# Kernel optimization log

Hardware: AMD Instinct MI355X
Metric: run time of the kernel (lower is better)

The kernel has to match this reference:

```python
import jax, jax.numpy as jnp
import numpy as np

NMS_THRE = 0.4
NEG = -1e30  # sentinel for sort key of suppressed boxes


def _iou_adjacency(boxes, nms_thre):
    # boxes: [N,4] in cxcywh -> xyxy, then dense IoU >= thre adjacency (no self loops)
    cx, cy, w, h = boxes[:, 0], boxes[:, 1], boxes[:, 2], boxes[:, 3]
    x1 = cx - w / 2
    y1 = cy - h / 2
    x2 = x1 + w
    y2 = y1 + h
    b = jnp.stack([x1, y1, x2, y2], axis=-1)  # [N,4]
    area = (x2 - x1) * (y2 - y1)
    lt = jnp.maximum(b[:, None, :2], b[None, :, :2])  # [N,N,2]
    rb = jnp.minimum(b[:, None, 2:], b[None, :, 2:])
    wh = jnp.clip(rb - lt, 0.0)
    inter = wh[..., 0] * wh[..., 1]
    iou = inter / (area[:, None] + area[None, :] - inter)
    n = boxes.shape[0]
    return (iou >= nms_thre) & (~jnp.eye(n, dtype=bool))


def _greedy_suppress(valid0, adj, scores):
    # Sequential greedy NMS over candidates in descending score order.
    # valid shrinks monotonically, and valid <= valid0 always, so clearing
    # neighbors via adj row exactly matches the torch loop (which only clears
    # neighbors that were initially valid -- already-false entries are no-ops).
    order = jnp.argsort(-scores)

    def body(k, valid):
        idx = order[k]
        return jnp.where(valid[idx], valid & (~adj[idx]), valid)

    return jax.lax.fori_loop(0, scores.shape[0], body, valid0)


def _per_class(pro_c, con_c, conf_c, adj):
    # scatter_max over adjacency: max of con over neighbors (0 if no neighbors,
    # matching torch_scatter's zero-init)
    adj_con = jnp.max(jnp.where(adj, con_c[None, :], 0.0), axis=1)
    valid0 = (pro_c >= conf_c) & (pro_c >= adj_con) & (pro_c >= con_c)
    return _greedy_suppress(valid0, adj, pro_c)


def _per_image(pro, con, boxes, scale, conf_thres):
    # pro/con: [N,C]; boxes: [N,4] cxcywh; scale: scalar; conf_thres: [C]
    adj = _iou_adjacency(boxes, NMS_THRE)
    survive = jax.vmap(_per_class, in_axes=(1, 1, 0, None))(pro, con, conf_thres, adj)  # [C,N]
    b = boxes * scale
    cx, cy, w, h = b[:, 0], b[:, 1], b[:, 2], b[:, 3]
    xyxy = jnp.stack([cx - 0.5 * w, cy - 0.5 * h, cx + 0.5 * w, cy + 0.5 * h], axis=-1)  # [N,4]
    scores = pro.T  # [C,N]
    C = scores.shape[0]
    bws = jnp.concatenate(
        [jnp.broadcast_to(xyxy[None], (C,) + xyxy.shape), scores[..., None]], axis=-1
    )  # [C,N,5]
    bws = bws * survive[..., None].astype(bws.dtype)  # zero out suppressed rows
    key = jnp.where(survive, scores, NEG)
    perm = jnp.argsort(-key, axis=1)  # per-class descending score order
    bws = jnp.take_along_axis(bws, perm[..., None], axis=1)
    mask = jnp.take_along_axis(survive, perm, axis=1)
    return bws, mask


def setup_inputs() -> dict:
    key = jax.random.key(0)
    k1, k2, k3, k4 = jax.random.split(key, 4)
    B, N, C = 4, 3600, 16
    return {
        "pro_max": jax.random.uniform(k1, (B, N, C), dtype=jnp.float32),
        "con_max": jax.random.uniform(k2, (B, N, C), dtype=jnp.float32),
        "pred_boxes": jax.random.uniform(k3, (B, N, 4), dtype=jnp.float32),
        "image_scales": jax.random.uniform(k4, (B,), dtype=jnp.float32),
        "conf_thres": jnp.zeros((C,), dtype=jnp.float32),
    }


def reference(pro_max, con_max, pred_boxes, image_scales, conf_thres):
    # Returns (boxes_with_scores [B,C,N,5] sorted per class by score desc,
    #          survive_mask [B,C,N] aligned with the sorted rows).
    return jax.vmap(_per_image, in_axes=(0, 0, 0, 0, None))(
        pro_max, con_max, pred_boxes, image_scales, conf_thres
    )
```

## Files before the change

kernel.cpp:

```cpp
#include <hip/hip_runtime.h>
#include <cstdint>

typedef unsigned long long u64;
typedef unsigned int u32;

#define B_ 4
#define N_ 3600
#define C_ 16
#define NW_ 57
#define NPAD_ 3648
#define RPW_ 4
#define RPB_ 16
#define HW0_ 1856
#define HW1_ 1792
#define CH_ 64
#define NT_ 512
#define NWV_ 8
#define RPWG_ 8

__global__ __launch_bounds__(256, 4) void k_adj(const float* __restrict__ boxes,
                                                const float* __restrict__ con,
                                                u64* __restrict__ adj,
                                                float* __restrict__ thr) {
#pragma clang fp contract(off)
    __shared__ float4 sbox[HW0_];
    const int tid  = threadIdx.x;
    const int lane = tid & 63;
    const int wv   = tid >> 6;
    const int g    = blockIdx.x;
    const int b    = g / (N_ / RPB_);
    const int r0   = (g % (N_ / RPB_)) * RPB_ + wv * RPW_;
    const size_t bN = (size_t)b * N_;

    float4 bi[RPW_];
    float  ai[RPW_];
#pragma unroll
    for (int r = 0; r < RPW_; ++r) {
        const float4 bx = reinterpret_cast<const float4*>(boxes)[bN + r0 + r];
        const float x1 = bx.x - bx.z * 0.5f;
        const float y1 = bx.y - bx.w * 0.5f;
        const float x2 = x1 + bx.z;
        const float y2 = y1 + bx.w;
        bi[r] = make_float4(x1, y1, x2, y2);
        ai[r] = (x2 - x1) * (y2 - y1);
    }
    const double MID = (double)0.4f - 0x1p-26;

    u64 row[RPW_];
#pragma unroll
    for (int r = 0; r < RPW_; ++r) row[r] = 0ull;

    int jbase = 0;
    for (int h = 0; h < 2; ++h) {
        const int cnt = h ? HW1_ : HW0_;
        __syncthreads();
        for (int jj = tid; jj < cnt; jj += 256) {
            const int j = jbase + jj;
            float x1 = 0.f, y1 = 0.f, x2 = 0.f, y2 = 0.f;
            if (j < N_) {
                const float4 bx = reinterpret_cast<const float4*>(boxes)[bN + j];
                x1 = bx.x - bx.z * 0.5f;
                y1 = bx.y - bx.w * 0.5f;
                x2 = x1 + bx.z;
                y2 = y1 + bx.w;
            }
            sbox[jj] = make_float4(x1, y1, x2, y2);
        }
        __syncthreads();

        const int twn = cnt >> 6;
        for (int tw = 0; tw < twn; ++tw) {
            const int tglob = (jbase >> 6) + tw;
            const int j     = jbase + tw * 64 + lane;
            const float4 bj = sbox[tw * 64 + lane];
            const float ajr = (bj.z - bj.x) * (bj.w - bj.y);
#pragma unroll
            for (int r = 0; r < RPW_; ++r) {
                const float ltx = fmaxf(bi[r].x, bj.x);
                const float lty = fmaxf(bi[r].y, bj.y);
                const float rbx = fminf(bi[r].z, bj.z);
                const float rby = fminf(bi[r].w, bj.w);
                const float whx = fmaxf(rbx - ltx, 0.0f);
                const float why = fmaxf(rby - lty, 0.0f);
                const float inter = whx * why;
                const float denom = (ai[r] + ajr) - inter;
                const int pred = ((double)inter > MID * (double)denom) && (j != r0 + r);
                const u64 m = __ballot(pred);
                if (lane == tglob) row[r] = m;
            }
        }
        jbase += cnt;
    }

#pragma unroll
    for (int r = 0; r < RPW_; ++r)
        if (lane < NW_) adj[(bN + r0 + r) * (size_t)NW_ + lane] = row[r];

#pragma unroll 1
    for (int r = 0; r < RPW_; ++r) {
        const int i = r0 + r;
        u64 w = row[r];
        float cm[C_];
#pragma unroll
        for (int k = 0; k < C_; ++k) cm[k] = 0.0f;

        while (w) {
            const int bit = __builtin_ctzll(w); w &= w - 1;
            const int j   = lane * 64 + bit;
            const float4* cp = reinterpret_cast<const float4*>(con + (bN + j) * C_);
            const float4 c0 = cp[0], c1 = cp[1], c2 = cp[2], c3 = cp[3];
            cm[0]  = fmaxf(cm[0],  c0.x); cm[1]  = fmaxf(cm[1],  c0.y);
            cm[2]  = fmaxf(cm[2],  c0.z); cm[3]  = fmaxf(cm[3],  c0.w);
            cm[4]  = fmaxf(cm[4],  c1.x); cm[5]  = fmaxf(cm[5],  c1.y);
            cm[6]  = fmaxf(cm[6],  c1.z); cm[7]  = fmaxf(cm[7],  c1.w);
            cm[8]  = fmaxf(cm[8],  c2.x); cm[9]  = fmaxf(cm[9],  c2.y);
            cm[10] = fmaxf(cm[10], c2.z); cm[11] = fmaxf(cm[11], c2.w);
            cm[12] = fmaxf(cm[12], c3.x); cm[13] = fmaxf(cm[13], c3.y);
            cm[14] = fmaxf(cm[14], c3.z); cm[15] = fmaxf(cm[15], c3.w);
        }

#pragma unroll
        for (int off = 1; off < 64; off <<= 1) {
#pragma unroll
            for (int k = 0; k < C_; ++k) cm[k] = fmaxf(cm[k], __shfl_xor(cm[k], off));
        }
        if (lane == 0) {
            const float4* cp = reinterpret_cast<const float4*>(con + (bN + i) * C_);
            const float4 c0 = cp[0], c1 = cp[1], c2 = cp[2], c3 = cp[3];
            float4* o = reinterpret_cast<float4*>(thr + (bN + i) * C_);
            o[0] = make_float4(fmaxf(cm[0],  c0.x), fmaxf(cm[1],  c0.y),
                               fmaxf(cm[2],  c0.z), fmaxf(cm[3],  c0.w));
            o[1] = make_float4(fmaxf(cm[4],  c1.x), fmaxf(cm[5],  c1.y),
                               fmaxf(cm[6],  c1.z), fmaxf(cm[7],  c1.w));
            o[2] = make_float4(fmaxf(cm[8],  c2.x), fmaxf(cm[9],  c2.y),
                               fmaxf(cm[10], c2.z), fmaxf(cm[11], c2.w));
            o[3] = make_float4(fmaxf(cm[12], c3.x), fmaxf(cm[13], c3.y),
                               fmaxf(cm[14], c3.z), fmaxf(cm[15], c3.w));
        }
    }
}

union OvT {
    u64 keys[NPAD_];
    u64 srows[2][CH_][NW_];
};

__global__ __launch_bounds__(NT_) void k_nms(const float* __restrict__ pro,
                                             const float* __restrict__ thr,
                                             const float* __restrict__ conf,
                                             const u64* __restrict__ adj,
                                             const float* __restrict__ boxes,
                                             const float* __restrict__ scales,
                                             float* __restrict__ out) {
#pragma clang fp contract(off)
    __shared__ OvT ov;
    __shared__ u32 sidx[NPAD_];
    __shared__ u64 sintra[CH_];
    __shared__ u64 vmask[NW_];
    __shared__ u64 s_accept;
    __shared__ u32 slist[NPAD_];
    __shared__ u32 s_T;
    __shared__ u32 s_S;
    const int tid  = threadIdx.x;
    const int lane = tid & 63;
    const int wv   = tid >> 6;
    const int bc   = blockIdx.x;
    const int b    = bc / C_, c = bc % C_;
    const size_t bN = (size_t)b * N_;
    const float cf = conf[c];

    if (tid == 0) s_T = 0;
    __syncthreads();

    for (int t = wv; t < NW_; t += NWV_) {
        const int i = t * 64 + lane;
        int pred = 0;
        u32 pk = 0;
        if (i < N_) {
            const size_t off = (bN + i) * C_ + c;
            const float p = pro[off];
            pred = (p >= cf) && (p >= thr[off]);
            const u32 pb = __float_as_uint(p);
            pk = pb ^ ((pb >> 31) ? 0xFFFFFFFFu : 0x80000000u);
        }
        const u64 bm = __ballot(pred);
        if (lane == 0) vmask[t] = bm;
        u32 base = 0;
        if (lane == 0 && bm) base = atomicAdd(&s_T, (u32)__popcll(bm));
        base = (u32)__shfl((int)base, 0);
        if (pred) ov.keys[base + (u32)__popcll(bm & ((1ull << lane) - 1ull))] =
            (((u64)(~pk)) << 32) | (u32)i;
    }
    __syncthreads();

    const int T = (int)s_T;
    for (int k = 0; k * NT_ < T; ++k) {
        const int x  = tid + k * NT_;
        const u64 kx = (x < T) ? ov.keys[x] : ~0ull;
        u32 rank = 0;
        for (int y = 0; y < T; ++y) rank += (ov.keys[y] < kx);
        if (x < T) sidx[rank] = (u32)(kx & 0xFFFFFFFFull);
    }
    __syncthreads();

#pragma unroll
    for (int rr = 0; rr < RPWG_; ++rr) {
        const int r = wv * RPWG_ + rr;
        const u32 idx = (r < T) ? sidx[r] : 0u;
        if (lane < NW_) ov.srows[0][r][lane] = adj[(bN + idx) * (size_t)NW_ + lane];
    }
    __syncthreads();

    u32 S = 0;
    const int NCH = (T + CH_ - 1) / CH_;
    for (int ch = 0; ch < NCH; ++ch) {
        const int cur = ch & 1, nxt = cur ^ 1;
        const int c0 = ch * CH_;
        const int cn = min(CH_, T - c0);
        const int havenext = (ch + 1 < NCH);

        u64 pre[RPWG_];
#pragma unroll
        for (int rr = 0; rr < RPWG_; ++rr) {
            const int r = wv * RPWG_ + rr;
            const int q = c0 + CH_ + r;
            const u32 idxn = (havenext && q < T) ? sidx[q] : 0u;
            pre[rr] = (havenext && lane < NW_)
                        ? adj[(bN + idxn) * (size_t)NW_ + lane] : 0ull;
        }
#pragma unroll
        for (int rr = 0; rr < RPWG_; ++rr) {
            const int r = wv * RPWG_ + rr;
            const u32 idxr = (c0 + r < T) ? sidx[c0 + r] : 0u;
            const u64 rj = ov.srows[cur][lane][idxr >> 6];
            const u64 ib = __ballot((lane < cn) && ((rj >> (idxr & 63)) & 1ull));
            if (lane == 0) sintra[r] = ib;
        }
        __syncthreads();

        if (wv == 0) {
            const u32 idxme = (c0 + lane < T) ? sidx[c0 + lane] : 0u;
            const u64 vm = vmask[idxme >> 6];
            u64 cv = __ballot((lane < cn) && ((vm >> (idxme & 63)) & 1ull));
            const u64 iv = sintra[lane];
            const u32 ivLo = (u32)iv, ivHi = (u32)(iv >> 32);
            u64 accept = 0ull;
            while (cv) {
                const int r = __builtin_ctzll(cv);
                accept |= 1ull << r;
                const u64 ir =
                    ((u64)(u32)__builtin_amdgcn_readlane((int)ivHi, r) << 32)
                  |  (u64)(u32)__builtin_amdgcn_readlane((int)ivLo, r);
                cv &= ~(ir | (1ull << r));
            }
            if (lane == 0) s_accept = accept;
            const u32 bitl = (u32)((accept >> lane) & 1ull);
            if (bitl) {
                const u32 pos = S + (u32)__popcll(accept & ((1ull << lane) - 1ull));
                slist[pos] = idxme;
            }
            S += (u32)__popcll(accept);
        }
        __syncthreads();

        const u64 ac = s_accept;
        u64 acc = 0ull;
#pragma unroll
        for (int rr = 0; rr < RPWG_; ++rr) {
            const int r = wv * RPWG_ + rr;
            if ((ac >> r) & 1ull)
                acc |= ov.srows[cur][r][min(lane, NW_ - 1)];
        }
        if (lane < NW_ && acc)
            atomicAnd(&vmask[lane], ~acc);
        if (havenext) {
#pragma unroll
            for (int rr = 0; rr < RPWG_; ++rr) {
                const int r = wv * RPWG_ + rr;
                if (lane < NW_) ov.srows[nxt][r][lane] = pre[rr];
            }
        }
        __syncthreads();
    }
    if (wv == 0 && lane == 0) s_S = S;
    __syncthreads();

    const int Sf = (int)s_S;
    const float s = scales[b];
    for (int r = tid; r < N_; r += NT_) {
        float o0 = 0.f, o1 = 0.f, o2 = 0.f, o3 = 0.f, o4 = 0.f, mk = 0.f;
        if (r < Sf) {
            const int idx = (int)slist[r];
            const float4 bx = reinterpret_cast<const float4*>(boxes)[bN + idx];
            const float scx = bx.x * s, scy = bx.y * s;
            const float sw  = bx.z * s, sh  = bx.w * s;
            o0 = scx - 0.5f * sw;
            o1 = scy - 0.5f * sh;
            o2 = scx + 0.5f * sw;
            o3 = scy + 0.5f * sh;
            o4 = pro[(bN + idx) * C_ + c];
            mk = 1.0f;
        }
        float* o = out + ((size_t)bc * N_ + r) * 5;
        o[0] = o0; o[1] = o1; o[2] = o2; o[3] = o3; o[4] = o4;
        out[(size_t)B_ * C_ * N_ * 5 + (size_t)bc * N_ + r] = mk;
    }
}

extern "C" void kernel_launch(void* const* d_in, const int* in_sizes, int n_in,
                              void* d_out, int out_size, void* d_ws, size_t ws_size,
                              hipStream_t stream) {
    const float* pro    = (const float*)d_in[0];
    const float* con    = (const float*)d_in[1];
    const float* boxes  = (const float*)d_in[2];
    const float* scales = (const float*)d_in[3];
    const float* conf   = (const float*)d_in[4];

    char* ws = (char*)d_ws;
    u64* adj = (u64*)ws;
    size_t off = (size_t)B_ * N_ * NW_ * sizeof(u64);
    float* thr = (float*)(ws + off);

    k_adj<<<B_ * N_ / RPB_, 256, 0, stream>>>(boxes, con, adj, thr);
    k_nms<<<B_ * C_,        NT_, 0, stream>>>(pro, thr, conf, adj, boxes,
                                              scales, (float*)d_out);
}
```

Before: 173.7 us.

## Exploit IoU symmetry: compute upper-triangular adjacency, mirror via bit transpose kernel

The adjacency kernel now computes only the 64-bit word tiles on or above the diagonal, since IoU is symmetric. A new kernel fills the lower triangle by transposing 64x64 bit blocks with shuffle-based butterfly swaps. The neighbor con-max reduction moves into its own kernel with one wavefront per row. This roughly halves the IoU work and drops shared-memory staging, at the cost of two extra launches and another pass over the adjacency matrix.

```diff
diff --git a/kernel.cpp b/kernel.cpp
--- a/kernel.cpp
+++ b/kernel.cpp
@@ -11,25 +11,23 @@
 #define NPAD_ 3648
 #define RPW_ 4
 #define RPB_ 16
-#define HW0_ 1856
-#define HW1_ 1792
+#define TPI_ 1596
 #define CH_ 64
 #define NT_ 512
 #define NWV_ 8
 #define RPWG_ 8
 
-__global__ __launch_bounds__(256, 4) void k_adj(const float* __restrict__ boxes,
-                                                const float* __restrict__ con,
-                                                u64* __restrict__ adj,
-                                                float* __restrict__ thr) {
+__global__ __launch_bounds__(256) void k_adj(const float* __restrict__ boxes,
+                                             u64* __restrict__ adj) {
 #pragma clang fp contract(off)
-    __shared__ float4 sbox[HW0_];
     const int tid  = threadIdx.x;
     const int lane = tid & 63;
     const int wv   = tid >> 6;
     const int g    = blockIdx.x;
     const int b    = g / (N_ / RPB_);
-    const int r0   = (g % (N_ / RPB_)) * RPB_ + wv * RPW_;
+    const int rg   = g % (N_ / RPB_);
+    const int r0   = rg * RPB_ + wv * RPW_;
+    const int w0   = rg >> 2;
     const size_t bN = (size_t)b * N_;
 
     float4 bi[RPW_];
@@ -50,93 +48,122 @@
 #pragma unroll
     for (int r = 0; r < RPW_; ++r) row[r] = 0ull;
 
-    int jbase = 0;
-    for (int h = 0; h < 2; ++h) {
-        const int cnt = h ? HW1_ : HW0_;
-        __syncthreads();
-        for (int jj = tid; jj < cnt; jj += 256) {
-            const int j = jbase + jj;
-            float x1 = 0.f, y1 = 0.f, x2 = 0.f, y2 = 0.f;
-            if (j < N_) {
-                const float4 bx = reinterpret_cast<const float4*>(boxes)[bN + j];
-                x1 = bx.x - bx.z * 0.5f;
-                y1 = bx.y - bx.w * 0.5f;
-                x2 = x1 + bx.z;
-                y2 = y1 + bx.w;
-            }
-            sbox[jj] = make_float4(x1, y1, x2, y2);
-        }
-        __syncthreads();
-
-        const int twn = cnt >> 6;
-        for (int tw = 0; tw < twn; ++tw) {
-            const int tglob = (jbase >> 6) + tw;
-            const int j     = jbase + tw * 64 + lane;
-            const float4 bj = sbox[tw * 64 + lane];
-            const float ajr = (bj.z - bj.x) * (bj.w - bj.y);
-#pragma unroll
-            for (int r = 0; r < RPW_; ++r) {
-                const float ltx = fmaxf(bi[r].x, bj.x);
-                const float lty = fmaxf(bi[r].y, bj.y);
-                const float rbx = fminf(bi[r].z, bj.z);
-                const float rby = fminf(bi[r].w, bj.w);
-                const float whx = fmaxf(rbx - ltx, 0.0f);
-                const float why = fmaxf(rby - lty, 0.0f);
-                const float inter = whx * why;
-                const float denom = (ai[r] + ajr) - inter;
-                const int pred = ((double)inter > MID * (double)denom) && (j != r0 + r);
-                const u64 m = __ballot(pred);
-                if (lane == tglob) row[r] = m;
-            }
-        }
-        jbase += cnt;
+    for (int tw = w0; tw < NW_; ++tw) {
+        const int j  = tw * 64 + lane;
+        const int jc = min(j, N_ - 1);
+        const float4 bx = reinterpret_cast<const float4*>(boxes)[bN + jc];
+        float x1 = bx.x - bx.z * 0.5f;
+        float y1 = bx.y - bx.w * 0.5f;
+        float x2 = x1 + bx.z;
+        float y2 = y1 + bx.w;
+        if (j >= N_) { x1 = 0.f; y1 = 0.f; x2 = 0.f; y2 = 0.f; }
+        const float ajr = (x2 - x1) * (y2 - y1);
+#pragma unroll
+        for (int r = 0; r < RPW_; ++r) {
+            const float ltx = fmaxf(bi[r].x, x1);
+            const float lty = fmaxf(bi[r].y, y1);
+            const float rbx = fminf(bi[r].z, x2);
+            const float rby = fminf(bi[r].w, y2);
+            const float whx = fmaxf(rbx - ltx, 0.0f);
+            const float why = fmaxf(rby - lty, 0.0f);
+            const float inter = whx * why;
+            const float denom = (ai[r] + ajr) - inter;
+            const int pred = ((double)inter > MID * (double)denom);
+            const u64 m = __ballot(pred);
+            if (lane == tw) row[r] = m;
+        }
     }
 
 #pragma unroll
     for (int r = 0; r < RPW_; ++r)
-        if (lane < NW_) adj[(bN + r0 + r) * (size_t)NW_ + lane] = row[r];
-
-#pragma unroll 1
-    for (int r = 0; r < RPW_; ++r) {
-        const int i = r0 + r;
-        u64 w = row[r];
-        float cm[C_];
-#pragma unroll
-        for (int k = 0; k < C_; ++k) cm[k] = 0.0f;
-
-        while (w) {
-            const int bit = __builtin_ctzll(w); w &= w - 1;
-            const int j   = lane * 64 + bit;
-            const float4* cp = reinterpret_cast<const float4*>(con + (bN + j) * C_);
-            const float4 c0 = cp[0], c1 = cp[1], c2 = cp[2], c3 = cp[3];
-            cm[0]  = fmaxf(cm[0],  c0.x); cm[1]  = fmaxf(cm[1],  c0.y);
-            cm[2]  = fmaxf(cm[2],  c0.z); cm[3]  = fmaxf(cm[3],  c0.w);
-            cm[4]  = fmaxf(cm[4],  c1.x); cm[5]  = fmaxf(cm[5],  c1.y);
-            cm[6]  = fmaxf(cm[6],  c1.z); cm[7]  = fmaxf(cm[7],  c1.w);
-            cm[8]  = fmaxf(cm[8],  c2.x); cm[9]  = fmaxf(cm[9],  c2.y);
-            cm[10] = fmaxf(cm[10], c2.z); cm[11] = fmaxf(cm[11], c2.w);
-            cm[12] = fmaxf(cm[12], c3.x); cm[13] = fmaxf(cm[13], c3.y);
-            cm[14] = fmaxf(cm[14], c3.z); cm[15] = fmaxf(cm[15], c3.w);
-        }
-
-#pragma unroll
-        for (int off = 1; off < 64; off <<= 1) {
-#pragma unroll
-            for (int k = 0; k < C_; ++k) cm[k] = fmaxf(cm[k], __shfl_xor(cm[k], off));
-        }
-        if (lane == 0) {
-            const float4* cp = reinterpret_cast<const float4*>(con + (bN + i) * C_);
-            const float4 c0 = cp[0], c1 = cp[1], c2 = cp[2], c3 = cp[3];
-            float4* o = reinterpret_cast<float4*>(thr + (bN + i) * C_);
-            o[0] = make_float4(fmaxf(cm[0],  c0.x), fmaxf(cm[1],  c0.y),
-                               fmaxf(cm[2],  c0.z), fmaxf(cm[3],  c0.w));
-            o[1] = make_float4(fmaxf(cm[4],  c1.x), fmaxf(cm[5],  c1.y),
-                               fmaxf(cm[6],  c1.z), fmaxf(cm[7],  c1.w));
-            o[2] = make_float4(fmaxf(cm[8],  c2.x), fmaxf(cm[9],  c2.y),
-                               fmaxf(cm[10], c2.z), fmaxf(cm[11], c2.w));
-            o[3] = make_float4(fmaxf(cm[12], c3.x), fmaxf(cm[13], c3.y),
-                               fmaxf(cm[14], c3.z), fmaxf(cm[15], c3.w));
-        }
+        if (lane == w0) row[r] &= ~(1ull << ((r0 + r) & 63));
+
+#pragma unroll
+    for (int r = 0; r < RPW_; ++r)
+        if (lane >= w0 && lane < NW_)
+            adj[(bN + r0 + r) * (size_t)NW_ + lane] = row[r];
+}
+
+__global__ __launch_bounds__(256) void k_tr(u64* __restrict__ adj) {
+    const int lane = threadIdx.x & 63;
+    const int wv   = threadIdx.x >> 6;
+    const int p    = blockIdx.x * 4 + wv;
+    const int b    = p / TPI_;
+    const int p2   = p % TPI_;
+    int wi = (int)((1.0f + sqrtf((float)(8 * p2 + 1))) * 0.5f);
+    while (wi * (wi - 1) / 2 > p2) --wi;
+    while ((wi + 1) * wi / 2 <= p2) ++wi;
+    const int wj = p2 - wi * (wi - 1) / 2;
+    const size_t bN = (size_t)b * N_;
+
+    u64 x = adj[(bN + wj * 64 + lane) * (size_t)NW_ + wi];
+
+    const u64 M[6] = {0x00000000FFFFFFFFull, 0x0000FFFF0000FFFFull,
+                      0x00FF00FF00FF00FFull, 0x0F0F0F0F0F0F0F0Full,
+                      0x3333333333333333ull, 0x5555555555555555ull};
+#pragma unroll
+    for (int si = 0; si < 6; ++si) {
+        const int s = 32 >> si;
+        const u64 m = M[si];
+        const u64 t = __shfl_xor(x, s);
+        x = ((lane & s) == 0) ? ((x & m) | ((t & m) << s))
+                              : ((x & ~m) | ((t & ~m) >> s));
+    }
+
+    const int rowi = wi * 64 + lane;
+    if (rowi < N_)
+        adj[(bN + rowi) * (size_t)NW_ + wj] = x;
+}
+
+__global__ __launch_bounds__(256) void k_acon(const u64* __restrict__ adj,
+                                              const float* __restrict__ con,
+                                              float* __restrict__ thr) {
+    const int tid  = threadIdx.x;
+    const int lane = tid & 63;
+    const int wv   = tid >> 6;
+    const int g    = blockIdx.x;
+    const int b    = g / (N_ / 4);
+    const int i    = (g % (N_ / 4)) * 4 + wv;
+    const size_t bN = (size_t)b * N_;
+
+    u64 w = (lane < NW_) ? adj[(bN + i) * (size_t)NW_ + lane] : 0ull;
+
+    float cm[C_];
+#pragma unroll
+    for (int k = 0; k < C_; ++k) cm[k] = 0.0f;
+
+    while (w) {
+        const int bit = __builtin_ctzll(w); w &= w - 1;
+        const int j   = lane * 64 + bit;
+        const float4* cp = reinterpret_cast<const float4*>(con + (bN + j) * C_);
+        const float4 c0 = cp[0], c1 = cp[1], c2 = cp[2], c3 = cp[3];
+        cm[0]  = fmaxf(cm[0],  c0.x); cm[1]  = fmaxf(cm[1],  c0.y);
+        cm[2]  = fmaxf(cm[2],  c0.z); cm[3]  = fmaxf(cm[3],  c0.w);
+        cm[4]  = fmaxf(cm[4],  c1.x); cm[5]  = fmaxf(cm[5],  c1.y);
+        cm[6]  = fmaxf(cm[6],  c1.z); cm[7]  = fmaxf(cm[7],  c1.w);
+        cm[8]  = fmaxf(cm[8],  c2.x); cm[9]  = fmaxf(cm[9],  c2.y);
+        cm[10] = fmaxf(cm[10], c2.z); cm[11] = fmaxf(cm[11], c2.w);
+        cm[12] = fmaxf(cm[12], c3.x); cm[13] = fmaxf(cm[13], c3.y);
+        cm[14] = fmaxf(cm[14], c3.z); cm[15] = fmaxf(cm[15], c3.w);
+    }
+
+#pragma unroll
+    for (int off = 1; off < 64; off <<= 1) {
+#pragma unroll
+        for (int k = 0; k < C_; ++k) cm[k] = fmaxf(cm[k], __shfl_xor(cm[k], off));
+    }
+    if (lane == 0) {
+        const float4* cp = reinterpret_cast<const float4*>(con + (bN + i) * C_);
+        const float4 c0 = cp[0], c1 = cp[1], c2 = cp[2], c3 = cp[3];
+        float4* o = reinterpret_cast<float4*>(thr + (bN + i) * C_);
+        o[0] = make_float4(fmaxf(cm[0],  c0.x), fmaxf(cm[1],  c0.y),
+                           fmaxf(cm[2],  c0.z), fmaxf(cm[3],  c0.w));
+        o[1] = make_float4(fmaxf(cm[4],  c1.x), fmaxf(cm[5],  c1.y),
+                           fmaxf(cm[6],  c1.z), fmaxf(cm[7],  c1.w));
+        o[2] = make_float4(fmaxf(cm[8],  c2.x), fmaxf(cm[9],  c2.y),
+                           fmaxf(cm[10], c2.z), fmaxf(cm[11], c2.w));
+        o[3] = make_float4(fmaxf(cm[12], c3.x), fmaxf(cm[13], c3.y),
+                           fmaxf(cm[14], c3.z), fmaxf(cm[15], c3.w));
     }
 }
 
@@ -321,7 +348,9 @@
     size_t off = (size_t)B_ * N_ * NW_ * sizeof(u64);
     float* thr = (float*)(ws + off);
 
-    k_adj<<<B_ * N_ / RPB_, 256, 0, stream>>>(boxes, con, adj, thr);
-    k_nms<<<B_ * C_,        NT_, 0, stream>>>(pro, thr, conf, adj, boxes,
-                                              scales, (float*)d_out);
-}
+    k_adj <<<B_ * N_ / RPB_,    256, 0, stream>>>(boxes, adj);
+    k_tr  <<<B_ * TPI_ / 4,     256, 0, stream>>>(adj);
+    k_acon<<<B_ * N_ / 4,       256, 0, stream>>>(adj, con, thr);
+    k_nms <<<B_ * C_,           NT_, 0, stream>>>(pro, thr, conf, adj, boxes,
+                                                  scales, (float*)d_out);
+}
```

Result: no change. 175.1 us (+0.8%).
